# Kernel optimization log

Measured on AMD Instinct MI355X. Metric: run time of the kernel, lower is better.

Reference implementation:

```python
import jax, jax.numpy as jnp
import numpy as np

N = 50000      # nodes
E = 800000     # edges (avg degree 16)
IN = 256       # in_dim
OUT = 128      # out_dim
H = 4          # heads
D = OUT // H   # head_dim = 32


def setup_inputs() -> dict:
    key = jax.random.key(0)
    k1, k2, k3, k4 = jax.random.split(key, 4)
    x = jax.random.normal(k1, (N, IN), dtype=jnp.float32)
    edge_index = jax.random.randint(k2, (2, E), 0, N, dtype=jnp.int32)
    W = jax.random.normal(k3, (OUT, IN), dtype=jnp.float32) * 0.05   # Linear(in_dim, out_dim, bias=False)
    a_w = jax.random.normal(k4, (2 * D,), dtype=jnp.float32) * 0.05  # Linear(2*head_dim, 1, bias=False)
    return {"x": x, "edge_index": edge_index, "W": W, "a_w": a_w}


def reference(x, edge_index, W, a_w):
    # Wx: [N, H, D]
    Wx = (x @ W.T).reshape(N, H, D)
    src, dst = edge_index[0], edge_index[1]
    # a([Wx_src, Wx_dst]) == Wx_src @ a_w[:D] + Wx_dst @ a_w[D:]; compute per-node then gather
    a_s, a_d = a_w[:D], a_w[D:]
    s_src = jnp.einsum('nhd,d->nh', Wx, a_s)  # [N, H]
    s_dst = jnp.einsum('nhd,d->nh', Wx, a_d)  # [N, H]
    e = jax.nn.leaky_relu(s_src[src] + s_dst[dst], negative_slope=0.2)  # [E, H]
    e_exp = jnp.exp(e)
    denom = jax.ops.segment_sum(e_exp, dst, num_segments=N)             # [N, H]
    alpha = e_exp / (denom[dst] + 1e-8)                                 # [E, H] (dropout=0 / eval)
    weighted = alpha[..., None] * Wx[src]                               # [E, H, D]
    out = jax.ops.segment_sum(weighted, dst, num_segments=N)            # [N, H, D]
    return jax.nn.elu(out.reshape(N, OUT))
```

## Files before the change

kernel.cpp:

```cpp
#include <hip/hip_runtime.h>
#include <math.h>

#define NN 50000
#define NE 800000
#define INF_ 256
#define OUTF 128
#define CAPB 64

typedef __attribute__((ext_vector_type(8))) __bf16 bf16x8;
typedef __attribute__((ext_vector_type(4))) float floatx4;

__device__ __forceinline__ unsigned short f2bf(float v) {
    unsigned int u = __float_as_uint(v);
    return (unsigned short)((u + 0x7FFFu + ((u >> 16) & 1u)) >> 16);
}
__device__ __forceinline__ float bf2f(unsigned short u) {
    return __uint_as_float(((unsigned int)u) << 16);
}

__global__ __launch_bounds__(256) void wsplit_kernel(
    const float* __restrict__ W, unsigned short* __restrict__ whi,
    unsigned short* __restrict__ wlo)
{
    int i = blockIdx.x * 256 + threadIdx.x;
    float v = W[i];
    unsigned short hb = f2bf(v);
    float lo = v - bf2f(hb);
    whi[i] = hb;
    wlo[i] = f2bf(lo);
}

#define GBM 64
#define XLD 40
#define WLD 40

__global__ __launch_bounds__(256) void gemm_s_kernel(
    const float* __restrict__ x, const unsigned short* __restrict__ whi,
    const unsigned short* __restrict__ wlo, const float* __restrict__ a_w,
    unsigned short* __restrict__ Wxh, float* __restrict__ s_src,
    float* __restrict__ s_dst)
{
    __shared__ __align__(16) unsigned short xhi[GBM * XLD];
    __shared__ __align__(16) unsigned short xlo[GBM * XLD];
    __shared__ __align__(16) unsigned short bhi[OUTF * WLD];
    __shared__ __align__(16) unsigned short blo[OUTF * WLD];
    const int t = threadIdx.x;
    const int w = t >> 6, lane = t & 63;
    const int g = lane >> 4, il = lane & 15;
    const int bm = blockIdx.x * GBM;

    floatx4 acc[4][2];
#pragma unroll
    for (int mt = 0; mt < 4; ++mt)
#pragma unroll
        for (int nt = 0; nt < 2; ++nt)
            acc[mt][nt] = (floatx4){0.f, 0.f, 0.f, 0.f};

    for (int kc = 0; kc < INF_; kc += 32) {
#pragma unroll
        for (int p = 0; p < 2; ++p) {
            int f = t + p * 256;
            int row = f >> 3, kq = (f & 7) * 4;
            int gr = bm + row;
            float4 v = make_float4(0.f, 0.f, 0.f, 0.f);
            if (gr < NN) v = *(const float4*)&x[(size_t)gr * INF_ + kc + kq];
            ushort4 hv, lv;
            hv.x = f2bf(v.x); lv.x = f2bf(v.x - bf2f(hv.x));
            hv.y = f2bf(v.y); lv.y = f2bf(v.y - bf2f(hv.y));
            hv.z = f2bf(v.z); lv.z = f2bf(v.z - bf2f(hv.z));
            hv.w = f2bf(v.w); lv.w = f2bf(v.w - bf2f(hv.w));
            *(ushort4*)&xhi[row * XLD + kq] = hv;
            *(ushort4*)&xlo[row * XLD + kq] = lv;
        }
#pragma unroll
        for (int p = 0; p < 4; ++p) {
            int f = t + p * 256;
            int col = f >> 3, kq = (f & 7) * 4;
            *(ushort4*)&bhi[col * WLD + kq] = *(const ushort4*)&whi[(size_t)col * INF_ + kc + kq];
            *(ushort4*)&blo[col * WLD + kq] = *(const ushort4*)&wlo[(size_t)col * INF_ + kc + kq];
        }
        __syncthreads();

        bf16x8 Bh0 = *(const bf16x8*)&bhi[(w * 32 + il) * WLD + g * 8];
        bf16x8 Bh1 = *(const bf16x8*)&bhi[(w * 32 + 16 + il) * WLD + g * 8];
        bf16x8 Bl0 = *(const bf16x8*)&blo[(w * 32 + il) * WLD + g * 8];
        bf16x8 Bl1 = *(const bf16x8*)&blo[(w * 32 + 16 + il) * WLD + g * 8];
#pragma unroll
        for (int mt = 0; mt < 4; ++mt) {
            bf16x8 Ah = *(const bf16x8*)&xhi[(mt * 16 + il) * XLD + g * 8];
            bf16x8 Al = *(const bf16x8*)&xlo[(mt * 16 + il) * XLD + g * 8];
            acc[mt][0] = __builtin_amdgcn_mfma_f32_16x16x32_bf16(Ah, Bh0, acc[mt][0], 0, 0, 0);
            acc[mt][0] = __builtin_amdgcn_mfma_f32_16x16x32_bf16(Al, Bh0, acc[mt][0], 0, 0, 0);
            acc[mt][0] = __builtin_amdgcn_mfma_f32_16x16x32_bf16(Ah, Bl0, acc[mt][0], 0, 0, 0);
            acc[mt][1] = __builtin_amdgcn_mfma_f32_16x16x32_bf16(Ah, Bh1, acc[mt][1], 0, 0, 0);
            acc[mt][1] = __builtin_amdgcn_mfma_f32_16x16x32_bf16(Al, Bh1, acc[mt][1], 0, 0, 0);
            acc[mt][1] = __builtin_amdgcn_mfma_f32_16x16x32_bf16(Ah, Bl1, acc[mt][1], 0, 0, 0);
        }
        __syncthreads();
    }

    const float as0 = a_w[il],      as1 = a_w[16 + il];
    const float ad0 = a_w[32 + il], ad1 = a_w[48 + il];
#pragma unroll
    for (int mt = 0; mt < 4; ++mt) {
#pragma unroll
        for (int r = 0; r < 4; ++r) {
            int row = bm + mt * 16 + g * 4 + r;
            float v0 = acc[mt][0][r], v1 = acc[mt][1][r];
            if (row < NN) {
                Wxh[(size_t)row * OUTF + w * 32 + il]      = f2bf(v0);
                Wxh[(size_t)row * OUTF + w * 32 + 16 + il] = f2bf(v1);
            }
            float ps = v0 * as0 + v1 * as1;
            float pd = v0 * ad0 + v1 * ad1;
            ps += __shfl_xor(ps, 1); ps += __shfl_xor(ps, 2);
            ps += __shfl_xor(ps, 4); ps += __shfl_xor(ps, 8);
            pd += __shfl_xor(pd, 1); pd += __shfl_xor(pd, 2);
            pd += __shfl_xor(pd, 4); pd += __shfl_xor(pd, 8);
            if (il == 0 && row < NN) {
                s_src[row * 4 + w] = ps;
                s_dst[row * 4 + w] = pd;
            }
        }
    }
}

__global__ void scatter_kernel(const int* __restrict__ src, const int* __restrict__ dst,
                               int* __restrict__ fill, int* __restrict__ colsrc) {
    int i = blockIdx.x * blockDim.x + threadIdx.x;
    if (i < NE) {
        int d = dst[i];
        int pos = atomicAdd(&fill[d], 1);
        if (pos < CAPB) colsrc[d * CAPB + pos] = src[i];
    }
}

__global__ __launch_bounds__(256) void gat_out_kernel(
    const unsigned short* __restrict__ Wxh, const float* __restrict__ s_src,
    const float* __restrict__ s_dst, const int* __restrict__ fill,
    const int* __restrict__ colsrc, float* __restrict__ out)
{
    __shared__ float lexp[4][CAPB * 4];
    __shared__ int   lsrc[4][CAPB];
    const int w = threadIdx.x >> 6;
    const int lane = threadIdx.x & 63;
    const int wid = (blockIdx.x << 2) + w;
    const int degr = fill[wid];
    const int deg = degr < CAPB ? degr : CAPB;
    const float4 sd = *(const float4*)&s_dst[(size_t)wid * 4];

    float e0 = 0.f, e1 = 0.f, e2 = 0.f, e3 = 0.f;
    int s = 0;
    if (lane < deg) {
        s = colsrc[wid * CAPB + lane];
        float4 ss = *(const float4*)&s_src[(size_t)s * 4];
        float t0 = ss.x + sd.x; t0 = t0 > 0.f ? t0 : 0.2f * t0; e0 = expf(t0);
        float t1 = ss.y + sd.y; t1 = t1 > 0.f ? t1 : 0.2f * t1; e1 = expf(t1);
        float t2 = ss.z + sd.z; t2 = t2 > 0.f ? t2 : 0.2f * t2; e2 = expf(t2);
        float t3 = ss.w + sd.w; t3 = t3 > 0.f ? t3 : 0.2f * t3; e3 = expf(t3);
    }
    float d0 = e0, d1 = e1, d2 = e2, d3 = e3;
#pragma unroll
    for (int o = 32; o > 0; o >>= 1) {
        d0 += __shfl_xor(d0, o);
        d1 += __shfl_xor(d1, o);
        d2 += __shfl_xor(d2, o);
        d3 += __shfl_xor(d3, o);
    }
    const float i0 = 1.f / (d0 + 1e-8f), i1 = 1.f / (d1 + 1e-8f);
    const float i2 = 1.f / (d2 + 1e-8f), i3 = 1.f / (d3 + 1e-8f);
    *(float4*)&lexp[w][lane * 4] = make_float4(e0 * i0, e1 * i1, e2 * i2, e3 * i3);
    lsrc[w][lane] = (lane < deg) ? (s << 8) : 0;
    __syncthreads();

    const int el = lane >> 5;
    const int fl = lane & 31;
    const int f = fl * 4;
    const int h = fl >> 3;
    const char* wbase = (const char*)Wxh + f * 2;

    float a0 = 0.f, a1 = 0.f, a2 = 0.f, a3 = 0.f;
    float b0 = 0.f, b1 = 0.f, b2 = 0.f, b3 = 0.f;
    for (int q = 0; q < deg; q += 4) {
        int o0 = lsrc[w][q + el];
        int o1 = lsrc[w][q + 2 + el];
        float al0 = lexp[w][(q + el) * 4 + h];
        float al1 = lexp[w][(q + 2 + el) * 4 + h];
        ushort4 u0 = *(const ushort4*)(wbase + o0);
        ushort4 u1 = *(const ushort4*)(wbase + o1);
        a0 = fmaf(al0, bf2f(u0.x), a0); a1 = fmaf(al0, bf2f(u0.y), a1);
        a2 = fmaf(al0, bf2f(u0.z), a2); a3 = fmaf(al0, bf2f(u0.w), a3);
        b0 = fmaf(al1, bf2f(u1.x), b0); b1 = fmaf(al1, bf2f(u1.y), b1);
        b2 = fmaf(al1, bf2f(u1.z), b2); b3 = fmaf(al1, bf2f(u1.w), b3);
    }
    a0 += b0; a1 += b1; a2 += b2; a3 += b3;
    a0 += __shfl_xor(a0, 32); a1 += __shfl_xor(a1, 32);
    a2 += __shfl_xor(a2, 32); a3 += __shfl_xor(a3, 32);
    if (el == 0) {
        a0 = a0 > 0.f ? a0 : expm1f(a0);
        a1 = a1 > 0.f ? a1 : expm1f(a1);
        a2 = a2 > 0.f ? a2 : expm1f(a2);
        a3 = a3 > 0.f ? a3 : expm1f(a3);
        *(float4*)&out[(size_t)wid * OUTF + f] = make_float4(a0, a1, a2, a3);
    }
}

extern "C" void kernel_launch(void* const* d_in, const int* in_sizes, int n_in,
                              void* d_out, int out_size, void* d_ws, size_t ws_size,
                              hipStream_t stream) {
    const float* x   = (const float*)d_in[0];
    const int*   ei  = (const int*)d_in[1];
    const float* W   = (const float*)d_in[2];
    const float* a_w = (const float*)d_in[3];
    const int* esrc = ei;
    const int* edst = ei + NE;
    float* out = (float*)d_out;

    char* ws = (char*)d_ws;
    size_t off = 0;
    auto alloc = [&](size_t bytes) -> char* {
        char* p = ws + off;
        off += (bytes + 255) & ~(size_t)255;
        return p;
    };
    unsigned short* Wxh = (unsigned short*)alloc((size_t)NN * OUTF * 2);
    unsigned short* whi = (unsigned short*)alloc((size_t)OUTF * INF_ * 2);
    unsigned short* wlo = (unsigned short*)alloc((size_t)OUTF * INF_ * 2);
    float* s_src  = (float*)alloc((size_t)NN * 4 * 4);
    float* s_dst  = (float*)alloc((size_t)NN * 4 * 4);
    int*   fill   = (int*)alloc((size_t)NN * 4);
    int*   colsrc = (int*)alloc((size_t)NN * CAPB * 4);

    hipMemsetAsync(fill, 0, (size_t)NN * 4, stream);

    wsplit_kernel<<<dim3((OUTF * INF_) / 256), dim3(256), 0, stream>>>(W, whi, wlo);
    gemm_s_kernel<<<dim3((NN + GBM - 1) / GBM), dim3(256), 0, stream>>>(
        x, whi, wlo, a_w, Wxh, s_src, s_dst);
    scatter_kernel<<<dim3((NE + 255) / 256), dim3(256), 0, stream>>>(
        esrc, edst, fill, colsrc);
    gat_out_kernel<<<dim3(NN / 4), dim3(256), 0, stream>>>(
        Wxh, s_src, s_dst, fill, colsrc, out);
}
```

Measured before the change: 208.0 us.

## Fuse edge scatter with weight split and store source indices as 16-bit

```diff
diff --git a/kernel.cpp b/kernel.cpp
--- a/kernel.cpp
+++ b/kernel.cpp
@@ -7,6 +7,11 @@
 #define OUTF 128
 #define CAPB 64
 
+#define SC_EPT 4
+#define SC_THREADS (NE / SC_EPT)
+#define SC_BLOCKS ((SC_THREADS + 255) / 256)
+#define WS_BLOCKS ((OUTF * INF_) / 256)
+
 typedef __attribute__((ext_vector_type(8))) __bf16 bf16x8;
 typedef __attribute__((ext_vector_type(4))) float floatx4;
 
@@ -18,16 +23,31 @@
     return __uint_as_float(((unsigned int)u) << 16);
 }
 
-__global__ __launch_bounds__(256) void wsplit_kernel(
+__global__ __launch_bounds__(256) void scatter_wsplit_kernel(
+    const int* __restrict__ src, const int* __restrict__ dst,
+    int* __restrict__ fill, unsigned short* __restrict__ colsrc,
     const float* __restrict__ W, unsigned short* __restrict__ whi,
     unsigned short* __restrict__ wlo)
 {
-    int i = blockIdx.x * 256 + threadIdx.x;
-    float v = W[i];
-    unsigned short hb = f2bf(v);
-    float lo = v - bf2f(hb);
-    whi[i] = hb;
-    wlo[i] = f2bf(lo);
+    const int b = blockIdx.x;
+    if (b < SC_BLOCKS) {
+        const int tid = b * 256 + threadIdx.x;
+        if (tid < SC_THREADS) {
+#pragma unroll
+            for (int p = 0; p < SC_EPT; ++p) {
+                int i = tid + p * SC_THREADS;
+                int d = dst[i];
+                int pos = atomicAdd(&fill[d], 1);
+                if (pos < CAPB) colsrc[d * CAPB + pos] = (unsigned short)src[i];
+            }
+        }
+    } else {
+        const int i = (b - SC_BLOCKS) * 256 + threadIdx.x;
+        float v = W[i];
+        unsigned short hb = f2bf(v);
+        whi[i] = hb;
+        wlo[i] = f2bf(v - bf2f(hb));
+    }
 }
 
 #define GBM 64
@@ -125,20 +145,10 @@
     }
 }
 
-__global__ void scatter_kernel(const int* __restrict__ src, const int* __restrict__ dst,
-                               int* __restrict__ fill, int* __restrict__ colsrc) {
-    int i = blockIdx.x * blockDim.x + threadIdx.x;
-    if (i < NE) {
-        int d = dst[i];
-        int pos = atomicAdd(&fill[d], 1);
-        if (pos < CAPB) colsrc[d * CAPB + pos] = src[i];
-    }
-}
-
 __global__ __launch_bounds__(256) void gat_out_kernel(
     const unsigned short* __restrict__ Wxh, const float* __restrict__ s_src,
     const float* __restrict__ s_dst, const int* __restrict__ fill,
-    const int* __restrict__ colsrc, float* __restrict__ out)
+    const unsigned short* __restrict__ colsrc, float* __restrict__ out)
 {
     __shared__ float lexp[4][CAPB * 4];
     __shared__ int   lsrc[4][CAPB];
@@ -229,15 +239,14 @@
     float* s_src  = (float*)alloc((size_t)NN * 4 * 4);
     float* s_dst  = (float*)alloc((size_t)NN * 4 * 4);
     int*   fill   = (int*)alloc((size_t)NN * 4);
-    int*   colsrc = (int*)alloc((size_t)NN * CAPB * 4);
+    unsigned short* colsrc = (unsigned short*)alloc((size_t)NN * CAPB * 2);
 
     hipMemsetAsync(fill, 0, (size_t)NN * 4, stream);
 
-    wsplit_kernel<<<dim3((OUTF * INF_) / 256), dim3(256), 0, stream>>>(W, whi, wlo);
+    scatter_wsplit_kernel<<<dim3(SC_BLOCKS + WS_BLOCKS), dim3(256), 0, stream>>>(
+        esrc, edst, fill, colsrc, W, whi, wlo);
     gemm_s_kernel<<<dim3((NN + GBM - 1) / GBM), dim3(256), 0, stream>>>(
         x, whi, wlo, a_w, Wxh, s_src, s_dst);
-    scatter_kernel<<<dim3((NE + 255) / 256), dim3(256), 0, stream>>>(
-        esrc, edst, fill, colsrc);
     gat_out_kernel<<<dim3(NN / 4), dim3(256), 0, stream>>>(
         Wxh, s_src, s_dst, fill, colsrc, out);
 }
```

Result: slower. 225.0 us (+8.1%).

## Merge W split, GEMM and edge scatter into one launch; store 16-bit indices

Applied to the files above, without the earlier changes.

```diff
diff --git a/kernel.cpp b/kernel.cpp
--- a/kernel.cpp
+++ b/kernel.cpp
@@ -7,6 +7,10 @@
 #define OUTF 128
 #define CAPB 64
 
+#define GBM 64
+#define GEMM_BLOCKS ((NN + GBM - 1) / GBM)
+#define SCAT_BLOCKS ((NE + 255) / 256)
+
 typedef __attribute__((ext_vector_type(8))) __bf16 bf16x8;
 typedef __attribute__((ext_vector_type(4))) float floatx4;
 
@@ -18,33 +22,32 @@
     return __uint_as_float(((unsigned int)u) << 16);
 }
 
-__global__ __launch_bounds__(256) void wsplit_kernel(
-    const float* __restrict__ W, unsigned short* __restrict__ whi,
-    unsigned short* __restrict__ wlo)
-{
-    int i = blockIdx.x * 256 + threadIdx.x;
-    float v = W[i];
-    unsigned short hb = f2bf(v);
-    float lo = v - bf2f(hb);
-    whi[i] = hb;
-    wlo[i] = f2bf(lo);
-}
-
-#define GBM 64
 #define XLD 40
 #define WLD 40
 
-__global__ __launch_bounds__(256) void gemm_s_kernel(
-    const float* __restrict__ x, const unsigned short* __restrict__ whi,
-    const unsigned short* __restrict__ wlo, const float* __restrict__ a_w,
-    unsigned short* __restrict__ Wxh, float* __restrict__ s_src,
-    float* __restrict__ s_dst)
+__global__ __launch_bounds__(256) void gemm_scatter_kernel(
+    const float* __restrict__ x, const float* __restrict__ W,
+    const float* __restrict__ a_w, unsigned short* __restrict__ Wxh,
+    float* __restrict__ s_src, float* __restrict__ s_dst,
+    const int* __restrict__ src, const int* __restrict__ dst,
+    int* __restrict__ fill, unsigned short* __restrict__ colsrc)
 {
     __shared__ __align__(16) unsigned short xhi[GBM * XLD];
     __shared__ __align__(16) unsigned short xlo[GBM * XLD];
     __shared__ __align__(16) unsigned short bhi[OUTF * WLD];
     __shared__ __align__(16) unsigned short blo[OUTF * WLD];
     const int t = threadIdx.x;
+
+    if (blockIdx.x >= GEMM_BLOCKS) {
+        int i = (blockIdx.x - GEMM_BLOCKS) * 256 + t;
+        if (i < NE) {
+            int d = dst[i];
+            int pos = atomicAdd(&fill[d], 1);
+            if (pos < CAPB) colsrc[d * CAPB + pos] = (unsigned short)src[i];
+        }
+        return;
+    }
+
     const int w = t >> 6, lane = t & 63;
     const int g = lane >> 4, il = lane & 15;
     const int bm = blockIdx.x * GBM;
@@ -76,8 +79,14 @@
         for (int p = 0; p < 4; ++p) {
             int f = t + p * 256;
             int col = f >> 3, kq = (f & 7) * 4;
-            *(ushort4*)&bhi[col * WLD + kq] = *(const ushort4*)&whi[(size_t)col * INF_ + kc + kq];
-            *(ushort4*)&blo[col * WLD + kq] = *(const ushort4*)&wlo[(size_t)col * INF_ + kc + kq];
+            float4 v = *(const float4*)&W[(size_t)col * INF_ + kc + kq];
+            ushort4 hv, lv;
+            hv.x = f2bf(v.x); lv.x = f2bf(v.x - bf2f(hv.x));
+            hv.y = f2bf(v.y); lv.y = f2bf(v.y - bf2f(hv.y));
+            hv.z = f2bf(v.z); lv.z = f2bf(v.z - bf2f(hv.z));
+            hv.w = f2bf(v.w); lv.w = f2bf(v.w - bf2f(hv.w));
+            *(ushort4*)&bhi[col * WLD + kq] = hv;
+            *(ushort4*)&blo[col * WLD + kq] = lv;
         }
         __syncthreads();
 
@@ -125,20 +134,10 @@
     }
 }
 
-__global__ void scatter_kernel(const int* __restrict__ src, const int* __restrict__ dst,
-                               int* __restrict__ fill, int* __restrict__ colsrc) {
-    int i = blockIdx.x * blockDim.x + threadIdx.x;
-    if (i < NE) {
-        int d = dst[i];
-        int pos = atomicAdd(&fill[d], 1);
-        if (pos < CAPB) colsrc[d * CAPB + pos] = src[i];
-    }
-}
-
 __global__ __launch_bounds__(256) void gat_out_kernel(
     const unsigned short* __restrict__ Wxh, const float* __restrict__ s_src,
     const float* __restrict__ s_dst, const int* __restrict__ fill,
-    const int* __restrict__ colsrc, float* __restrict__ out)
+    const unsigned short* __restrict__ colsrc, float* __restrict__ out)
 {
     __shared__ float lexp[4][CAPB * 4];
     __shared__ int   lsrc[4][CAPB];
@@ -224,20 +223,15 @@
         return p;
     };
     unsigned short* Wxh = (unsigned short*)alloc((size_t)NN * OUTF * 2);
-    unsigned short* whi = (unsigned short*)alloc((size_t)OUTF * INF_ * 2);
-    unsigned short* wlo = (unsigned short*)alloc((size_t)OUTF * INF_ * 2);
     float* s_src  = (float*)alloc((size_t)NN * 4 * 4);
     float* s_dst  = (float*)alloc((size_t)NN * 4 * 4);
     int*   fill   = (int*)alloc((size_t)NN * 4);
-    int*   colsrc = (int*)alloc((size_t)NN * CAPB * 4);
+    unsigned short* colsrc = (unsigned short*)alloc((size_t)NN * CAPB * 2);
 
     hipMemsetAsync(fill, 0, (size_t)NN * 4, stream);
 
-    wsplit_kernel<<<dim3((OUTF * INF_) / 256), dim3(256), 0, stream>>>(W, whi, wlo);
-    gemm_s_kernel<<<dim3((NN + GBM - 1) / GBM), dim3(256), 0, stream>>>(
-        x, whi, wlo, a_w, Wxh, s_src, s_dst);
-    scatter_kernel<<<dim3((NE + 255) / 256), dim3(256), 0, stream>>>(
-        esrc, edst, fill, colsrc);
+    gemm_scatter_kernel<<<dim3(GEMM_BLOCKS + SCAT_BLOCKS), dim3(256), 0, stream>>>(
+        x, W, a_w, Wxh, s_src, s_dst, esrc, edst, fill, colsrc);
     gat_out_kernel<<<dim3(NN / 4), dim3(256), 0, stream>>>(
         Wxh, s_src, s_dst, fill, colsrc, out);
 }
```

After: 185.9 us. -10.6%, faster.
